# Optimization experiments

Measured on AMD Instinct MI355X. Metric: run time of the kernel, lower is better.

## Reference

```python
import jax, jax.numpy as jnp
import numpy as np

D_MODEL = 1024
NUM_HEADS = 16
HEAD_DIM = D_MODEL // NUM_HEADS
THETA = 10000.0
BATCH = 2
SEQ = 2048


def _apply_rope(x, positions):
    # x: (b, h, s, hd), positions: (b, s) int
    hd = x.shape[-1]
    inv_freq = 1.0 / (THETA ** (jnp.arange(0, hd, 2, dtype=jnp.float32) / hd))  # (hd/2,)
    ang = positions.astype(jnp.float32)[:, None, :, None] * inv_freq  # (b,1,s,hd/2)
    cos, sin = jnp.cos(ang), jnp.sin(ang)
    x1 = x[..., 0::2]
    x2 = x[..., 1::2]
    r1 = x1 * cos - x2 * sin
    r2 = x1 * sin + x2 * cos
    return jnp.stack([r1, r2], axis=-1).reshape(x.shape)


def setup_inputs() -> dict:
    key = jax.random.key(0)
    ks = jax.random.split(key, 5)
    scale = 1.0 / np.sqrt(D_MODEL)
    x = jax.random.normal(ks[0], (BATCH, SEQ, D_MODEL), dtype=jnp.float32)
    token_positions = jnp.broadcast_to(jnp.arange(SEQ, dtype=jnp.int32), (BATCH, SEQ))
    W_q = jax.random.normal(ks[1], (D_MODEL, D_MODEL), dtype=jnp.float32) * scale
    W_k = jax.random.normal(ks[2], (D_MODEL, D_MODEL), dtype=jnp.float32) * scale
    W_v = jax.random.normal(ks[3], (D_MODEL, D_MODEL), dtype=jnp.float32) * scale
    W_o = jax.random.normal(ks[4], (D_MODEL, D_MODEL), dtype=jnp.float32) * scale
    return {"x": x, "token_positions": token_positions, "W_q": W_q, "W_k": W_k, "W_v": W_v, "W_o": W_o}


def reference(x, token_positions, W_q, W_k, W_v, W_o):
    b, s, _ = x.shape
    h, hd = NUM_HEADS, HEAD_DIM
    # bias-free Linear: y = x @ W^T, W: (out, in)
    def proj(W):
        return jnp.einsum('bsd,ed->bse', x, W).reshape(b, s, h, hd).transpose(0, 2, 1, 3)
    Q = _apply_rope(proj(W_q), token_positions)
    K = _apply_rope(proj(W_k), token_positions)
    V = proj(W_v)
    scores = jnp.einsum('bhqd,bhkd->bhqk', Q, K) / jnp.sqrt(jnp.float32(hd))
    causal = jnp.triu(jnp.full((s, s), -jnp.inf, dtype=scores.dtype), k=1)
    attn = jax.nn.softmax(scores + causal, axis=-1)
    Z = jnp.einsum('bhqk,bhkd->bhqd', attn, V)
    Z = Z.transpose(0, 2, 1, 3).reshape(b, s, h * hd)
    return jnp.einsum('bse,de->bsd', Z, W_o)
```

## Files before the change

kernel.cpp:

```cpp
#include <hip/hip_runtime.h>
#include <hip/hip_bf16.h>


#define BATCH 2
#define SEQ   2048
#define NH    16
#define HD    64
#define DM    1024
#define MTOT  (BATCH*SEQ)

typedef __attribute__((ext_vector_type(8))) short bf16x8;
typedef __attribute__((ext_vector_type(4))) float f32x4;
typedef __attribute__((ext_vector_type(4))) unsigned int u32x4;
typedef unsigned short u16;
typedef unsigned int   u32;

__device__ __forceinline__ float b2f(u16 h){ return __uint_as_float(((u32)h) << 16); }
__device__ __forceinline__ u16 f2b(float f){
  u32 u = __float_as_uint(f);
  u32 r = (u + 0x7FFFu + ((u >> 16) & 1u)) >> 16;
  return (u16)r;
}
__device__ __forceinline__ u16 cvt1(float f){
  __hip_bfloat16 h = __float2bfloat16(f);
  return *reinterpret_cast<u16*>(&h);
}
__device__ __forceinline__ u32 pk2(float lo, float hi){
  return (u32)cvt1(lo) | ((u32)cvt1(hi) << 16);
}
__device__ __forceinline__ f32x4 mfma16(bf16x8 a, bf16x8 b, f32x4 c){
  return __builtin_amdgcn_mfma_f32_16x16x32_bf16(a, b, c, 0, 0, 0);
}
__device__ __forceinline__ void gload_lds16(const u16* g, u16* l){
  __builtin_amdgcn_global_load_lds((const __attribute__((address_space(1))) unsigned int*)g,
                                   (__attribute__((address_space(3))) unsigned int*)l, 16, 0, 0);
}

__global__ __launch_bounds__(256) void cvt_all(const float* __restrict__ x,
    const float* __restrict__ wq, const float* __restrict__ wk,
    const float* __restrict__ wv, const float* __restrict__ wo,
    u16* __restrict__ xb, u16* __restrict__ wb)
{
  const long NX = (long)MTOT * DM;
  const long NW = (long)DM * DM;
  const long tot4 = (NX + 4*NW) >> 2;
  for (long t = (long)blockIdx.x*blockDim.x + threadIdx.x; t < tot4;
       t += (long)gridDim.x*blockDim.x){
    long e = t << 2;
    const float* s; u16* d;
    if (e < NX){ s = x + e; d = xb + e; }
    else {
      long j = e - NX; int z = (int)(j >> 20);
      const float* ws = (z==0)?wq:(z==1)?wk:(z==2)?wv:wo;
      s = ws + (j & (NW-1)); d = wb + j;
    }
    float4 v = *(const float4*)s;
    u32 lo = (u32)f2b(v.x) | ((u32)f2b(v.y) << 16);
    u32 hi = (u32)f2b(v.z) | ((u32)f2b(v.w) << 16);
    uint2 o; o.x = lo; o.y = hi;
    *(uint2*)d = o;
  }
}

__global__ __launch_bounds__(256) void rope_table(float2* __restrict__ tab){
  int t = blockIdx.x*blockDim.x + threadIdx.x;
  if (t >= SEQ*32) return;
  int s = t >> 5, i = t & 31;
  float inv = 1.0f / powf(10000.0f, (float)i * (1.0f/32.0f));
  float a = (float)s * inv;
  tab[t] = make_float2(cosf(a), sinf(a));
}

__device__ __forceinline__ void gemm128_core(const u16* __restrict__ A, const u16* __restrict__ B,
    int mbase, int nbase, u16* Alds, u16* Blds, f32x4 acc[4][4])
{
  const int tid = threadIdx.x;
  const int w = tid >> 6, l = tid & 63, g = l >> 4, c = l & 15;
  const int wr = (w >> 1)*64, wc = (w & 1)*64;
  const int srow = l >> 3;
  const int scol = ((l & 7) ^ srow)*8;
  const u16* Ag = A + (long)(mbase + w*32 + srow)*DM + scol;
  const u16* Bg = B + (long)(nbase + w*32 + srow)*DM + scol;
  u16* Alb = Alds + w*2048;
  u16* Blb = Blds + w*2048;

  for (int k0 = 0; k0 < DM; k0 += 64){
    __syncthreads();
    #pragma unroll
    for (int i = 0; i < 4; i++){
      gload_lds16(Ag + k0 + (long)(8*i)*DM, Alb + i*512);
      gload_lds16(Bg + k0 + (long)(8*i)*DM, Blb + i*512);
    }
    __syncthreads();
    #pragma unroll
    for (int ks = 0; ks < 2; ks++){
      bf16x8 af[4], bfr[4];
      #pragma unroll
      for (int mi = 0; mi < 4; mi++){
        int row = wr + mi*16 + c;
        af[mi] = *(const bf16x8*)&Alds[row*64 + (((ks*4 + g) ^ (row & 7))*8)];
      }
      #pragma unroll
      for (int nj = 0; nj < 4; nj++){
        int row = wc + nj*16 + c;
        bfr[nj] = *(const bf16x8*)&Blds[row*64 + (((ks*4 + g) ^ (row & 7))*8)];
      }
      #pragma unroll
      for (int mi = 0; mi < 4; mi++)
        #pragma unroll
        for (int nj = 0; nj < 4; nj++)
          acc[mi][nj] = mfma16(af[mi], bfr[nj], acc[mi][nj]);
    }
  }
}

__global__ __launch_bounds__(256) void gemm_qkv(const u16* __restrict__ xb,
                                                const u16* __restrict__ wb,
                                                u16* __restrict__ qkvr)
{
  __shared__ u16 Alds[128*64];
  __shared__ u16 Blds[128*64];
  const int z = blockIdx.z;
  const u16* Bm = wb + (long)z * DM * DM;
  u16* C = qkvr + (long)z * MTOT * DM;
  const int nbase = blockIdx.x*128, mbase = blockIdx.y*128;
  const int w = threadIdx.x >> 6, l = threadIdx.x & 63, g = l >> 4, c = l & 15;
  const int wr = (w >> 1)*64, wc = (w & 1)*64;
  f32x4 acc[4][4] = {};
  gemm128_core(xb, Bm, mbase, nbase, Alds, Blds, acc);
  #pragma unroll
  for (int mi = 0; mi < 4; mi++)
    #pragma unroll
    for (int nj = 0; nj < 4; nj++)
      #pragma unroll
      for (int r = 0; r < 4; r++){
        int row = mbase + wr + mi*16 + 4*g + r;
        int col = nbase + wc + nj*16 + c;
        C[(long)row*DM + col] = f2b(acc[mi][nj][r]);
      }
}

__global__ __launch_bounds__(256) void gemm_out(const u16* __restrict__ Zb,
                                                const u16* __restrict__ wob,
                                                float* __restrict__ out)
{
  __shared__ u16 Alds[128*64];
  __shared__ u16 Blds[128*64];
  const int nbase = blockIdx.x*128, mbase = blockIdx.y*128;
  const int w = threadIdx.x >> 6, l = threadIdx.x & 63, g = l >> 4, c = l & 15;
  const int wr = (w >> 1)*64, wc = (w & 1)*64;
  f32x4 acc[4][4] = {};
  gemm128_core(Zb, wob, mbase, nbase, Alds, Blds, acc);
  #pragma unroll
  for (int mi = 0; mi < 4; mi++)
    #pragma unroll
    for (int nj = 0; nj < 4; nj++)
      #pragma unroll
      for (int r = 0; r < 4; r++){
        int row = mbase + wr + mi*16 + 4*g + r;
        int col = nbase + wc + nj*16 + c;
        out[(long)row*DM + col] = acc[mi][nj][r];
      }
}

__global__ __launch_bounds__(256) void rope_scatter(const u16* __restrict__ qkvr,
    u16* __restrict__ Qd, u16* __restrict__ Kd, u16* __restrict__ Vt,
    const float2* __restrict__ tab, const int* __restrict__ pos)
{
  int st = blockIdx.x, h = blockIdx.y, b = blockIdx.z;
  int s0 = st*64;
  const u16* Qraw = qkvr;
  const u16* Kraw = qkvr + (long)MTOT*DM;
  const u16* Vraw = qkvr + 2L*MTOT*DM;

  for (int t = threadIdx.x; t < 64*32; t += 256){
    int sl = t >> 5, i = t & 31;
    int s = s0 + sl;
    int p = pos[b*SEQ + s];
    if (p < 0) p = 0; if (p >= SEQ) p = SEQ - 1;
    float2 cs = tab[p*32 + i];
    long inoff  = (long)(b*SEQ + s)*DM + h*HD + 2*i;
    long outoff = ((long)(b*NH + h)*SEQ + s)*HD + 2*i;
    u32 qe = *(const u32*)(Qraw + inoff);
    float x1 = b2f((u16)(qe & 0xffff)), x2 = b2f((u16)(qe >> 16));
    float r1 = x1*cs.x - x2*cs.y;
    float r2 = x1*cs.y + x2*cs.x;
    *(u32*)(Qd + outoff) = (u32)f2b(r1) | ((u32)f2b(r2) << 16);
    u32 ke = *(const u32*)(Kraw + inoff);
    x1 = b2f((u16)(ke & 0xffff)); x2 = b2f((u16)(ke >> 16));
    r1 = x1*cs.x - x2*cs.y;
    r2 = x1*cs.y + x2*cs.x;
    *(u32*)(Kd + outoff) = (u32)f2b(r1) | ((u32)f2b(r2) << 16);
  }

  __shared__ u16 vt[64][65];
  for (int t = threadIdx.x; t < 64*8; t += 256){
    int sl = t >> 3, ch = (t & 7)*8;
    bf16x8 v = *(const bf16x8*)(Vraw + (long)(b*SEQ + s0 + sl)*DM + h*HD + ch);
    #pragma unroll
    for (int j = 0; j < 8; j++) vt[sl][ch + j] = (u16)v[j];
  }
  __syncthreads();
  for (int t = threadIdx.x; t < 64*8; t += 256){
    int d = t >> 3, ch = (t & 7)*8;
    bf16x8 v;
    #pragma unroll
    for (int j = 0; j < 8; j++) v[j] = (short)vt[ch + j][d];
    *(bf16x8*)(Vt + ((long)(b*NH + h)*HD + d)*SEQ + s0 + ch) = v;
  }
}

__device__ __forceinline__ int kperm(int a){
  return (a & 32) | ((a & 4) << 2) | ((a & 24) >> 1) | (a & 3);
}

__global__ __launch_bounds__(512) void attn(const u16* __restrict__ Q, const u16* __restrict__ K,
                                            const u16* __restrict__ Vt, u16* __restrict__ Z)
{
  const int qt = 15 - (int)blockIdx.x;
  const int h = blockIdx.y, b = blockIdx.z;
  const int qbase = qt*128;
  const int tid = threadIdx.x, w = tid >> 6, l = tid & 63, g = l >> 4, c = l & 15;
  const int qrow = qbase + w*16;
  const u16* Qp = Q  + ((long)(b*NH + h)*SEQ + qrow)*HD;
  const u16* Kp = K  + (long)(b*NH + h)*SEQ*HD;
  const u16* Vp = Vt + (long)(b*NH + h)*HD*SEQ;

  __shared__ u16 K_lds[2][64][64];
  __shared__ u16 V_lds[2][64][64];

  bf16x8 qf0 = *(const bf16x8*)(Qp + c*HD + g*8);
  bf16x8 qf1 = *(const bf16x8*)(Qp + c*HD + 32 + g*8);

  const int srow0 = tid >> 3, sch = tid & 7;
  const int kpr0 = kperm(srow0);

  f32x4 accz[4] = {};
  float m = -1e30f, lsum = 0.f;
  const int cswz = c & 7;

  bf16x8 kr, vr;
  kr = *(const bf16x8*)(Kp + (long)srow0*HD + sch*8);
  vr = *(const bf16x8*)(Vp + (long)srow0*SEQ + sch*8);
  *(bf16x8*)&K_lds[0][kpr0][(sch ^ (kpr0 & 7))*8] = kr;
  *(bf16x8*)&V_lds[0][srow0][(sch ^ (srow0 & 7))*8] = vr;

  const int ntiles = 2*qt + 2;
  int cur = 0;
  for (int t = 0; t < ntiles; ++t){
    const int kbase = t*64;
    __syncthreads();

    if (t < ntiles-1){
      const int nb = kbase + 64;
      kr = *(const bf16x8*)(Kp + (long)(nb + srow0)*HD + sch*8);
      vr = *(const bf16x8*)(Vp + (long)srow0*SEQ + nb + sch*8);
    }

    f32x4 s[4];
    __builtin_amdgcn_s_setprio(1);
    #pragma unroll
    for (int sub = 0; sub < 4; sub++){
      int row = sub*16 + c;
      bf16x8 ka0 = *(const bf16x8*)&K_lds[cur][row][((0+g) ^ cswz)*8];
      bf16x8 ka1 = *(const bf16x8*)&K_lds[cur][row][((4+g) ^ cswz)*8];
      f32x4 z4 = {};
      z4 = mfma16(ka0, qf0, z4);
      z4 = mfma16(ka1, qf1, z4);
      s[sub] = z4;
    }
    __builtin_amdgcn_s_setprio(0);

    const bool edge = (kbase + 63 > qrow);
    const int q = qrow + c;
    #pragma unroll
    for (int sub = 0; sub < 4; sub++)
      #pragma unroll
      for (int r = 0; r < 4; r++){
        float v = s[sub][r]*0.125f;
        if (edge){
          int key = kbase + ((sub >> 1) << 5) + 8*g + ((sub & 1) << 2) + r;
          if (key > q) v = -1e30f;
        }
        s[sub][r] = v;
      }

    float tmax = s[0][0];
    #pragma unroll
    for (int sub = 0; sub < 4; sub++)
      #pragma unroll
      for (int r = 0; r < 4; r++) tmax = fmaxf(tmax, s[sub][r]);
    tmax = fmaxf(tmax, __shfl_xor(tmax, 16));
    tmax = fmaxf(tmax, __shfl_xor(tmax, 32));

    if (!__all(tmax <= m + 8.f)){
      float nm = fmaxf(m, tmax);
      float f = __expf(m - nm);
      m = nm;
      lsum *= f;
      float f_bc[4];
      #pragma unroll
      for (int r = 0; r < 4; r++) f_bc[r] = __shfl(f, 4*g + r);
      #pragma unroll
      for (int dt = 0; dt < 4; dt++)
        #pragma unroll
        for (int r = 0; r < 4; r++) accz[dt][r] *= f_bc[r];
    }

    float psum = 0.f;
    #pragma unroll
    for (int sub = 0; sub < 4; sub++)
      #pragma unroll
      for (int r = 0; r < 4; r++){
        float e = __expf(s[sub][r] - m);
        s[sub][r] = e;
        psum += e;
      }
    psum += __shfl_xor(psum, 16);
    psum += __shfl_xor(psum, 32);
    lsum += psum;

    u32x4 p0, p1;
    p0[0] = pk2(s[0][0], s[0][1]); p0[1] = pk2(s[0][2], s[0][3]);
    p0[2] = pk2(s[1][0], s[1][1]); p0[3] = pk2(s[1][2], s[1][3]);
    p1[0] = pk2(s[2][0], s[2][1]); p1[1] = pk2(s[2][2], s[2][3]);
    p1[2] = pk2(s[3][0], s[3][1]); p1[3] = pk2(s[3][2], s[3][3]);
    bf16x8 pf0 = __builtin_bit_cast(bf16x8, p0);
    bf16x8 pf1 = __builtin_bit_cast(bf16x8, p1);

    __builtin_amdgcn_s_setprio(1);
    #pragma unroll
    for (int dt = 0; dt < 4; dt++){
      int vrow = dt*16 + c;
      bf16x8 vf0 = *(const bf16x8*)&V_lds[cur][vrow][((0+g) ^ cswz)*8];
      bf16x8 vf1 = *(const bf16x8*)&V_lds[cur][vrow][((4+g) ^ cswz)*8];
      accz[dt] = mfma16(pf0, vf0, accz[dt]);
      accz[dt] = mfma16(pf1, vf1, accz[dt]);
    }
    __builtin_amdgcn_s_setprio(0);

    if (t < ntiles-1){
      int nx = cur ^ 1;
      *(bf16x8*)&K_lds[nx][kpr0][(sch ^ (kpr0 & 7))*8] = kr;
      *(bf16x8*)&V_lds[nx][srow0][(sch ^ (srow0 & 7))*8] = vr;
      cur = nx;
    }
  }

  float lsum_bc[4];
  #pragma unroll
  for (int r = 0; r < 4; r++) lsum_bc[r] = __shfl(lsum, 4*g + r);
  #pragma unroll
  for (int dt = 0; dt < 4; dt++)
    #pragma unroll
    for (int r = 0; r < 4; r++){
      float zv = accz[dt][r] / lsum_bc[r];
      int row = qrow + 4*g + r;
      int col = dt*16 + c;
      Z[(long)(b*SEQ + row)*DM + h*HD + col] = cvt1(zv);
    }
}

extern "C" void kernel_launch(void* const* d_in, const int* in_sizes, int n_in,
                              void* d_out, int out_size, void* d_ws, size_t ws_size,
                              hipStream_t stream)
{
  const float* x  = (const float*)d_in[0];
  const int*   pos= (const int*)d_in[1];
  const float* wq = (const float*)d_in[2];
  const float* wk = (const float*)d_in[3];
  const float* wv = (const float*)d_in[4];
  const float* wo = (const float*)d_in[5];
  float* out = (float*)d_out;

  const long NX = (long)MTOT*DM;
  const long NW = (long)DM*DM;
  char* p = (char*)d_ws;
  u16* xb   = (u16*)p;  p += NX*2;
  u16* wb   = (u16*)p;  p += 4*NW*2;
  u16* qkvr = (u16*)p;  p += 3*NX*2;
  u16* Qd   = (u16*)p;  p += NX*2;
  u16* Kd   = (u16*)p;  p += NX*2;
  u16* Vt   = (u16*)p;  p += NX*2;
  u16* Zb   = (u16*)p;  p += NX*2;
  float2* tab = (float2*)p; p += (long)SEQ*32*sizeof(float2);
  (void)ws_size; (void)n_in; (void)in_sizes; (void)out_size;

  hipLaunchKernelGGL(cvt_all,     dim3(2048),      dim3(256), 0, stream, x, wq, wk, wv, wo, xb, wb);
  hipLaunchKernelGGL(rope_table,  dim3(256),       dim3(256), 0, stream, tab);
  hipLaunchKernelGGL(gemm_qkv,    dim3(8,32,3),    dim3(256), 0, stream, xb, wb, qkvr);
  hipLaunchKernelGGL(rope_scatter,dim3(32,16,2),   dim3(256), 0, stream, qkvr, Qd, Kd, Vt, tab, pos);
  hipLaunchKernelGGL(attn,        dim3(16,16,2),   dim3(512), 0, stream, Qd, Kd, Vt, Zb);
  hipLaunchKernelGGL(gemm_out,    dim3(8,32),      dim3(256), 0, stream, Zb, wb + 3*NW, out);
}
```

Baseline: 142.4 us.

## Split attention KV range across two blocks and merge with combine kernel

```diff
diff --git a/kernel.cpp b/kernel.cpp
--- a/kernel.cpp
+++ b/kernel.cpp
@@ -215,9 +215,11 @@
 }
 
 __global__ __launch_bounds__(512) void attn(const u16* __restrict__ Q, const u16* __restrict__ K,
-                                            const u16* __restrict__ Vt, u16* __restrict__ Z)
-{
-  const int qt = 15 - (int)blockIdx.x;
+                                            const u16* __restrict__ Vt,
+                                            u16* __restrict__ Opart, float2* __restrict__ ML)
+{
+  const int qt = 15 - ((int)blockIdx.x >> 1);
+  const int half = blockIdx.x & 1;
   const int h = blockIdx.y, b = blockIdx.z;
   const int qbase = qt*128;
   const int tid = threadIdx.x, w = tid >> 6, l = tid & 63, g = l >> 4, c = l & 15;
@@ -238,108 +240,113 @@
   f32x4 accz[4] = {};
   float m = -1e30f, lsum = 0.f;
   const int cswz = c & 7;
+  const float SC = 0.125f * 1.44269504089f;
+
+  const int tstart = half*(qt + 1);
+  const int tend   = tstart + qt + 1;
 
   bf16x8 kr, vr;
-  kr = *(const bf16x8*)(Kp + (long)srow0*HD + sch*8);
-  vr = *(const bf16x8*)(Vp + (long)srow0*SEQ + sch*8);
+  kr = *(const bf16x8*)(Kp + (long)(tstart*64 + srow0)*HD + sch*8);
+  vr = *(const bf16x8*)(Vp + (long)srow0*SEQ + tstart*64 + sch*8);
   *(bf16x8*)&K_lds[0][kpr0][(sch ^ (kpr0 & 7))*8] = kr;
   *(bf16x8*)&V_lds[0][srow0][(sch ^ (srow0 & 7))*8] = vr;
 
-  const int ntiles = 2*qt + 2;
   int cur = 0;
-  for (int t = 0; t < ntiles; ++t){
+  for (int t = tstart; t < tend; ++t){
     const int kbase = t*64;
     __syncthreads();
 
-    if (t < ntiles-1){
+    if (t < tend-1){
       const int nb = kbase + 64;
       kr = *(const bf16x8*)(Kp + (long)(nb + srow0)*HD + sch*8);
       vr = *(const bf16x8*)(Vp + (long)srow0*SEQ + nb + sch*8);
     }
 
-    f32x4 s[4];
-    __builtin_amdgcn_s_setprio(1);
-    #pragma unroll
-    for (int sub = 0; sub < 4; sub++){
-      int row = sub*16 + c;
-      bf16x8 ka0 = *(const bf16x8*)&K_lds[cur][row][((0+g) ^ cswz)*8];
-      bf16x8 ka1 = *(const bf16x8*)&K_lds[cur][row][((4+g) ^ cswz)*8];
-      f32x4 z4 = {};
-      z4 = mfma16(ka0, qf0, z4);
-      z4 = mfma16(ka1, qf1, z4);
-      s[sub] = z4;
-    }
-    __builtin_amdgcn_s_setprio(0);
-
-    const bool edge = (kbase + 63 > qrow);
-    const int q = qrow + c;
-    #pragma unroll
-    for (int sub = 0; sub < 4; sub++)
-      #pragma unroll
-      for (int r = 0; r < 4; r++){
-        float v = s[sub][r]*0.125f;
-        if (edge){
-          int key = kbase + ((sub >> 1) << 5) + 8*g + ((sub & 1) << 2) + r;
-          if (key > q) v = -1e30f;
+    if (kbase <= qrow + 15){
+      f32x4 s[4];
+      __builtin_amdgcn_s_setprio(1);
+      #pragma unroll
+      for (int sub = 0; sub < 4; sub++){
+        int row = sub*16 + c;
+        bf16x8 ka0 = *(const bf16x8*)&K_lds[cur][row][((0+g) ^ cswz)*8];
+        bf16x8 ka1 = *(const bf16x8*)&K_lds[cur][row][((4+g) ^ cswz)*8];
+        f32x4 z4 = {};
+        z4 = mfma16(ka0, qf0, z4);
+        z4 = mfma16(ka1, qf1, z4);
+        s[sub] = z4;
+      }
+      __builtin_amdgcn_s_setprio(0);
+
+      const bool edge = (kbase + 63 > qrow);
+      const int q = qrow + c;
+      #pragma unroll
+      for (int sub = 0; sub < 4; sub++)
+        #pragma unroll
+        for (int r = 0; r < 4; r++){
+          float v = s[sub][r]*SC;
+          if (edge){
+            int key = kbase + ((sub >> 1) << 5) + 8*g + ((sub & 1) << 2) + r;
+            if (key > q) v = -1e30f;
+          }
+          s[sub][r] = v;
         }
-        s[sub][r] = v;
-      }
-
-    float tmax = s[0][0];
-    #pragma unroll
-    for (int sub = 0; sub < 4; sub++)
-      #pragma unroll
-      for (int r = 0; r < 4; r++) tmax = fmaxf(tmax, s[sub][r]);
-    tmax = fmaxf(tmax, __shfl_xor(tmax, 16));
-    tmax = fmaxf(tmax, __shfl_xor(tmax, 32));
-
-    if (!__all(tmax <= m + 8.f)){
-      float nm = fmaxf(m, tmax);
-      float f = __expf(m - nm);
-      m = nm;
-      lsum *= f;
-      float f_bc[4];
-      #pragma unroll
-      for (int r = 0; r < 4; r++) f_bc[r] = __shfl(f, 4*g + r);
-      #pragma unroll
-      for (int dt = 0; dt < 4; dt++)
-        #pragma unroll
-        for (int r = 0; r < 4; r++) accz[dt][r] *= f_bc[r];
-    }
-
-    float psum = 0.f;
-    #pragma unroll
-    for (int sub = 0; sub < 4; sub++)
-      #pragma unroll
-      for (int r = 0; r < 4; r++){
-        float e = __expf(s[sub][r] - m);
-        s[sub][r] = e;
-        psum += e;
-      }
-    psum += __shfl_xor(psum, 16);
-    psum += __shfl_xor(psum, 32);
-    lsum += psum;
-
-    u32x4 p0, p1;
-    p0[0] = pk2(s[0][0], s[0][1]); p0[1] = pk2(s[0][2], s[0][3]);
-    p0[2] = pk2(s[1][0], s[1][1]); p0[3] = pk2(s[1][2], s[1][3]);
-    p1[0] = pk2(s[2][0], s[2][1]); p1[1] = pk2(s[2][2], s[2][3]);
-    p1[2] = pk2(s[3][0], s[3][1]); p1[3] = pk2(s[3][2], s[3][3]);
-    bf16x8 pf0 = __builtin_bit_cast(bf16x8, p0);
-    bf16x8 pf1 = __builtin_bit_cast(bf16x8, p1);
-
-    __builtin_amdgcn_s_setprio(1);
-    #pragma unroll
-    for (int dt = 0; dt < 4; dt++){
-      int vrow = dt*16 + c;
-      bf16x8 vf0 = *(const bf16x8*)&V_lds[cur][vrow][((0+g) ^ cswz)*8];
-      bf16x8 vf1 = *(const bf16x8*)&V_lds[cur][vrow][((4+g) ^ cswz)*8];
-      accz[dt] = mfma16(pf0, vf0, accz[dt]);
-      accz[dt] = mfma16(pf1, vf1, accz[dt]);
-    }
-    __builtin_amdgcn_s_setprio(0);
-
-    if (t < ntiles-1){
+
+      float tmax = s[0][0];
+      #pragma unroll
+      for (int sub = 0; sub < 4; sub++)
+        #pragma unroll
+        for (int r = 0; r < 4; r++) tmax = fmaxf(tmax, s[sub][r]);
+      tmax = fmaxf(tmax, __shfl_xor(tmax, 16));
+      tmax = fmaxf(tmax, __shfl_xor(tmax, 32));
+
+      if (!__all(tmax <= m + 8.f)){
+        float nm = fmaxf(m, tmax);
+        float f = exp2f(m - nm);
+        m = nm;
+        lsum *= f;
+        float f_bc[4];
+        #pragma unroll
+        for (int r = 0; r < 4; r++) f_bc[r] = __shfl(f, 4*g + r);
+        #pragma unroll
+        for (int dt = 0; dt < 4; dt++)
+          #pragma unroll
+          for (int r = 0; r < 4; r++) accz[dt][r] *= f_bc[r];
+      }
+
+      float psum = 0.f;
+      #pragma unroll
+      for (int sub = 0; sub < 4; sub++)
+        #pragma unroll
+        for (int r = 0; r < 4; r++){
+          float e = exp2f(s[sub][r] - m);
+          s[sub][r] = e;
+          psum += e;
+        }
+      psum += __shfl_xor(psum, 16);
+      psum += __shfl_xor(psum, 32);
+      lsum += psum;
+
+      u32x4 p0, p1;
+      p0[0] = pk2(s[0][0], s[0][1]); p0[1] = pk2(s[0][2], s[0][3]);
+      p0[2] = pk2(s[1][0], s[1][1]); p0[3] = pk2(s[1][2], s[1][3]);
+      p1[0] = pk2(s[2][0], s[2][1]); p1[1] = pk2(s[2][2], s[2][3]);
+      p1[2] = pk2(s[3][0], s[3][1]); p1[3] = pk2(s[3][2], s[3][3]);
+      bf16x8 pf0 = __builtin_bit_cast(bf16x8, p0);
+      bf16x8 pf1 = __builtin_bit_cast(bf16x8, p1);
+
+      __builtin_amdgcn_s_setprio(1);
+      #pragma unroll
+      for (int dt = 0; dt < 4; dt++){
+        int vrow = dt*16 + c;
+        bf16x8 vf0 = *(const bf16x8*)&V_lds[cur][vrow][((0+g) ^ cswz)*8];
+        bf16x8 vf1 = *(const bf16x8*)&V_lds[cur][vrow][((4+g) ^ cswz)*8];
+        accz[dt] = mfma16(pf0, vf0, accz[dt]);
+        accz[dt] = mfma16(pf1, vf1, accz[dt]);
+      }
+      __builtin_amdgcn_s_setprio(0);
+    }
+
+    if (t < tend-1){
       int nx = cur ^ 1;
       *(bf16x8*)&K_lds[nx][kpr0][(sch ^ (kpr0 & 7))*8] = kr;
       *(bf16x8*)&V_lds[nx][srow0][(sch ^ (srow0 & 7))*8] = vr;
@@ -347,18 +354,47 @@
     }
   }
 
-  float lsum_bc[4];
-  #pragma unroll
-  for (int r = 0; r < 4; r++) lsum_bc[r] = __shfl(lsum, 4*g + r);
+  const int pbase = (((b*NH + h)*16 + qt)*2 + half);
+  if (g == 0)
+    ML[pbase*128 + w*16 + c] = make_float2(m, lsum);
+  u16* Op = Opart + (long)pbase*(128*64);
   #pragma unroll
   for (int dt = 0; dt < 4; dt++)
     #pragma unroll
-    for (int r = 0; r < 4; r++){
-      float zv = accz[dt][r] / lsum_bc[r];
-      int row = qrow + 4*g + r;
-      int col = dt*16 + c;
-      Z[(long)(b*SEQ + row)*DM + h*HD + col] = cvt1(zv);
-    }
+    for (int r = 0; r < 4; r++)
+      Op[(w*16 + 4*g + r)*64 + dt*16 + c] = cvt1(accz[dt][r]);
+}
+
+__global__ __launch_bounds__(256) void attn_combine(const u16* __restrict__ Opart,
+                                                    const float2* __restrict__ ML,
+                                                    u16* __restrict__ Z)
+{
+  const int qt = blockIdx.x, h = blockIdx.y, b = blockIdx.z;
+  const int p0 = (((b*NH + h)*16 + qt)*2 + 0), p1 = p0 + 1;
+  const int row = threadIdx.x >> 1;
+  const int d0  = (threadIdx.x & 1)*32;
+  float2 ml0 = ML[p0*128 + row];
+  float2 ml1 = ML[p1*128 + row];
+  float M = fmaxf(ml0.x, ml1.x);
+  float w0 = exp2f(ml0.x - M), w1 = exp2f(ml1.x - M);
+  float inv = 1.f / (ml0.y*w0 + ml1.y*w1);
+  float a0 = w0*inv, a1 = w1*inv;
+  const u16* o0 = Opart + ((long)p0*128 + row)*64 + d0;
+  const u16* o1 = Opart + ((long)p1*128 + row)*64 + d0;
+  const int s = qt*128 + row;
+  u16* zp = Z + (long)(b*SEQ + s)*DM + h*HD + d0;
+  #pragma unroll
+  for (int j = 0; j < 4; j++){
+    bf16x8 va = *(const bf16x8*)(o0 + j*8);
+    bf16x8 vb = *(const bf16x8*)(o1 + j*8);
+    bf16x8 ov;
+    #pragma unroll
+    for (int e = 0; e < 8; e++){
+      float z = b2f((u16)va[e])*a0 + b2f((u16)vb[e])*a1;
+      ov[e] = (short)cvt1(z);
+    }
+    *(bf16x8*)(zp + j*8) = ov;
+  }
 }
 
 extern "C" void kernel_launch(void* const* d_in, const int* in_sizes, int n_in,
@@ -384,12 +420,15 @@
   u16* Vt   = (u16*)p;  p += NX*2;
   u16* Zb   = (u16*)p;  p += NX*2;
   float2* tab = (float2*)p; p += (long)SEQ*32*sizeof(float2);
+  u16* Opart = (u16*)p;  p += 2L*NX*2;
+  float2* ML = (float2*)p; p += 1024L*128*sizeof(float2);
   (void)ws_size; (void)n_in; (void)in_sizes; (void)out_size;
 
   hipLaunchKernelGGL(cvt_all,     dim3(2048),      dim3(256), 0, stream, x, wq, wk, wv, wo, xb, wb);
   hipLaunchKernelGGL(rope_table,  dim3(256),       dim3(256), 0, stream, tab);
   hipLaunchKernelGGL(gemm_qkv,    dim3(8,32,3),    dim3(256), 0, stream, xb, wb, qkvr);
   hipLaunchKernelGGL(rope_scatter,dim3(32,16,2),   dim3(256), 0, stream, qkvr, Qd, Kd, Vt, tab, pos);
-  hipLaunchKernelGGL(attn,        dim3(16,16,2),   dim3(512), 0, stream, Qd, Kd, Vt, Zb);
+  hipLaunchKernelGGL(attn,        dim3(32,16,2),   dim3(512), 0, stream, Qd, Kd, Vt, Opart, ML);
+  hipLaunchKernelGGL(attn_combine,dim3(16,16,2),   dim3(256), 0, stream, Opart, ML, Zb);
   hipLaunchKernelGGL(gemm_out,    dim3(8,32),      dim3(256), 0, stream, Zb, wb + 3*NW, out);
 }
```

After: 159.5 us. 1.12x slower.
